# Optimization experiments

Measured on AMD Instinct MI355X. Metric: run time of the kernel, lower is better.

## Reference

```python
import jax, jax.numpy as jnp
import numpy as np

EMB_DIM = 128
WALK_LEN = 40
WINDOW = 5
NEG_SIZE = 5
NEG_WEIGHT = 1.0
NUM_NODES = 1_000_000
BATCH = 512


def _pair_indices(walk_length=WALK_LEN, window_size=WINDOW):
    # replicates the idx_list_src / idx_list_dst construction in __init__
    src, dst = [], []
    for i in range(walk_length):
        for j in range(max(0, i - window_size), i):
            src.append(j); dst.append(i)
        for j in range(i + 1, min(walk_length, i + 1 + window_size)):
            src.append(j); dst.append(i)
    return np.asarray(src, dtype=np.int64), np.asarray(dst, dtype=np.int64)

_SRC, _DST = _pair_indices()  # each has 370 entries
NUM_PAIRS = _SRC.shape[0]


def setup_inputs() -> dict:
    key = jax.random.key(0)
    k1, k2, k3, k4 = jax.random.split(key, 4)
    batch_walk = jax.random.randint(k1, (BATCH, WALK_LEN), 0, NUM_NODES, dtype=jnp.int64)
    neg_idx_dst = jax.random.randint(k2, (BATCH * NUM_PAIRS * NEG_SIZE,), 0, BATCH * WALK_LEN, dtype=jnp.int64)
    init_range = 1.0 / EMB_DIM
    node_embed = jax.random.normal(k3, (NUM_NODES, EMB_DIM), dtype=jnp.float32) * init_range
    context_embed = jax.random.normal(k4, (NUM_NODES, EMB_DIM), dtype=jnp.float32) * init_range
    return {"batch_walk": batch_walk, "neg_idx_dst": neg_idx_dst,
            "node_embed": node_embed, "context_embed": context_embed}


def reference(batch_walk, neg_idx_dst, node_embed, context_embed):
    B = batch_walk.shape[0]
    flat_walk = batch_walk.reshape(-1)                      # [B*L]
    batch_node = node_embed[flat_walk]                      # [B*L, D]
    batch_ctx = context_embed[flat_walk]                    # [B*L, D]

    offsets = (jnp.arange(B, dtype=jnp.int64) * WALK_LEN)[:, None]
    idx_src = (offsets + jnp.asarray(_SRC)[None, :]).reshape(-1)  # [B*370]
    idx_dst = (offsets + jnp.asarray(_DST)[None, :]).reshape(-1)  # [B*370]

    pos_src = batch_node[idx_src]
    pos_dst = batch_ctx[idx_dst]
    pos_score = jnp.clip(jnp.sum(pos_src * pos_dst, axis=1), -6.0, 6.0)
    pos_loss = jnp.mean(-jax.nn.log_sigmoid(pos_score))

    neg_idx_src = jnp.repeat(idx_dst, NEG_SIZE)             # [B*370*NEG]
    neg_src = batch_node[neg_idx_src]
    neg_dst = batch_ctx[neg_idx_dst]
    neg_score = jnp.clip(jnp.sum(neg_src * neg_dst, axis=1), -6.0, 6.0)
    neg_loss = jnp.mean(-jax.nn.log_sigmoid(-neg_score)) * NEG_SIZE * NEG_WEIGHT

    return pos_loss + neg_loss
```

## Files before the change

### kernel.cpp

```cpp
#include <hip/hip_runtime.h>
#include <hip/hip_fp16.h>

#define WALK_LEN 40
#define WINDOW   5
#define NPAIRS   370
#define BATCHSZ  512
#define NEGK     5
#define NPOS     (BATCHSZ * NPAIRS)
#define EMB      128
#define NQ       (BATCHSZ * WALK_LEN)
#define THREADS  512
#define GROUPS   (THREADS / 8)
#define HALFP    185
#define NBLOCKS  (BATCHSZ * 2)

struct PairTab { short src[NPAIRS]; short dst[NPAIRS]; };

constexpr PairTab make_pairs() {
    PairTab t{};
    int k = 0;
    for (int i = 0; i < WALK_LEN; ++i) {
        int lo = (i - WINDOW > 0) ? (i - WINDOW) : 0;
        for (int j = lo; j < i; ++j) { t.src[k] = (short)j; t.dst[k] = (short)i; ++k; }
        int hi = (i + 1 + WINDOW < WALK_LEN) ? (i + 1 + WINDOW) : WALK_LEN;
        for (int j = i + 1; j < hi; ++j) { t.src[k] = (short)j; t.dst[k] = (short)i; ++k; }
    }
    return t;
}

__constant__ PairTab g_pairs = make_pairs();

template <int CTRL>
__device__ __forceinline__ float dpp_add(float x) {
    int y = __builtin_amdgcn_update_dpp(0, __float_as_int(x), CTRL, 0xF, 0xF, true);
    return x + __int_as_float(y);
}
__device__ __forceinline__ float grp8_sum(float d) {
    d = dpp_add<0xB1>(d);
    d = dpp_add<0x4E>(d);
    d = dpp_add<0x141>(d);
    return d;
}

__device__ __forceinline__ float h2dot(uint4 A0, uint4 A1, uint4 C0, uint4 C1) {
    const __half2* a0 = (const __half2*)&A0;
    const __half2* a1 = (const __half2*)&A1;
    const __half2* c0 = (const __half2*)&C0;
    const __half2* c1 = (const __half2*)&C1;
    __half2 h0 = __float2half2_rn(0.f);
    __half2 h1 = __float2half2_rn(0.f);
    #pragma unroll
    for (int i = 0; i < 4; ++i) {
        h0 = __hfma2(a0[i], c0[i], h0);
        h1 = __hfma2(a1[i], c1[i], h1);
    }
    const __half2 hs = __hadd2(h0, h1);
    return __low2float(hs) + __high2float(hs);
}

__device__ __forceinline__ float clip6(float x) {
    return fminf(6.f, fmaxf(-6.f, x));
}

__global__ __launch_bounds__(256) void dw_gather(
    const int*   __restrict__ walk,
    const float* __restrict__ nodeE,
    const float* __restrict__ ctxE,
    unsigned short* __restrict__ dN,
    unsigned short* __restrict__ dC,
    float* __restrict__ out)
{
    if (blockIdx.x == 0 && threadIdx.x == 0) out[0] = 0.f;
    int idx = blockIdx.x * 256 + threadIdx.x;
    const int is_ctx = (idx >= NQ * 32);
    if (is_ctx) idx -= NQ * 32;
    const int q = idx >> 5, c = idx & 31;
    const int row = walk[q];
    const float* src = (is_ctx ? ctxE : nodeE) + (size_t)row * EMB;
    const float4 v = *((const float4*)src + c);
    ushort4 o;
    o.x = __half_as_ushort(__float2half(v.x));
    o.y = __half_as_ushort(__float2half(v.y));
    o.z = __half_as_ushort(__float2half(v.z));
    o.w = __half_as_ushort(__float2half(v.w));
    unsigned short* dst = (is_ctx ? dC : dN) + (size_t)q * EMB;
    *((ushort4*)dst + c) = o;
}

#define SLOT_DECL(S)                                                        \
    const int  jj##S = (S) * GROUPS + grp;                                  \
    const int  j##S  = jbase + ((jj##S < HALFP) ? jj##S : 0);               \
    const int* nb##S = negdst + ((size_t)b * NPAIRS + j##S) * NEGK;         \
    const int  qa##S = nb##S[0], qb##S = nb##S[1], qc##S = nb##S[2],        \
               qd##S = nb##S[3], qe##S = nb##S[4];                          \
    const uint4* ga##S = (const uint4*)(dC + (size_t)qa##S * EMB);          \
    const uint4* gb##S = (const uint4*)(dC + (size_t)qb##S * EMB);          \
    const uint4* gc##S = (const uint4*)(dC + (size_t)qc##S * EMB);          \
    const uint4* gd##S = (const uint4*)(dC + (size_t)qd##S * EMB);          \
    const uint4* ge##S = (const uint4*)(dC + (size_t)qe##S * EMB);          \
    const uint4 xa0##S = ga##S[lane8], xa1##S = ga##S[lane8 + 8];           \
    const uint4 xb0##S = gb##S[lane8], xb1##S = gb##S[lane8 + 8];           \
    const uint4 xc0##S = gc##S[lane8], xc1##S = gc##S[lane8 + 8];           \
    const uint4 xd0##S = gd##S[lane8], xd1##S = gd##S[lane8 + 8];           \
    const uint4 xe0##S = ge##S[lane8], xe1##S = ge##S[lane8 + 8];

#define SLOT_COMPUTE(S)                                                     \
    if (jj##S < HALFP) {                                                    \
        const int sj = g_pairs.src[j##S];                                   \
        const int dj = g_pairs.dst[j##S];                                   \
        const uint4* rN = (const uint4*)(sN + sj * 64);                     \
        const uint4* rC = (const uint4*)(sC + dj * 64);                     \
        const uint4* rS = (const uint4*)(sN + dj * 64);                     \
        const uint4 a0 = rN[lane8], a1 = rN[lane8 + 8];                     \
        const uint4 c0 = rC[lane8], c1 = rC[lane8 + 8];                     \
        const uint4 n0 = rS[lane8], n1 = rS[lane8 + 8];                     \
        const float sp = clip6(grp8_sum(h2dot(a0, a1, c0, c1)));            \
        const float s0 = clip6(grp8_sum(h2dot(n0, n1, xa0##S, xa1##S)));    \
        const float s1 = clip6(grp8_sum(h2dot(n0, n1, xb0##S, xb1##S)));    \
        const float s2 = clip6(grp8_sum(h2dot(n0, n1, xc0##S, xc1##S)));    \
        const float s3 = clip6(grp8_sum(h2dot(n0, n1, xd0##S, xd1##S)));    \
        const float s4 = clip6(grp8_sum(h2dot(n0, n1, xe0##S, xe1##S)));    \
        \
        const float p0 = (1.f + __expf(-sp)) * (1.f + __expf(s0));          \
        const float p1 = (1.f + __expf(s1))  * (1.f + __expf(s2));          \
        const float p2 = (1.f + __expf(s3))  * (1.f + __expf(s4));          \
        acc += __logf(p0 * p1 * p2);                                        \
    }

__global__ __launch_bounds__(THREADS, 2) void dw_score(
    const int* __restrict__ negdst,
    const unsigned short* __restrict__ dN,
    const unsigned short* __restrict__ dC,
    float* __restrict__ out)
{
    __shared__ unsigned int sN[WALK_LEN * 64];
    __shared__ unsigned int sC[WALK_LEN * 64];
    __shared__ float wsum[THREADS / 64];

    const int b    = blockIdx.x >> 1;
    const int half = blockIdx.x & 1;
    const int tid  = threadIdx.x;

    {
        const uint4* srcN = (const uint4*)(dN + (size_t)b * WALK_LEN * EMB);
        const uint4* srcC = (const uint4*)(dC + (size_t)b * WALK_LEN * EMB);
        for (int u = tid; u < WALK_LEN * 16; u += THREADS) {
            ((uint4*)sN)[u] = srcN[u];
            ((uint4*)sC)[u] = srcC[u];
        }
    }
    __syncthreads();

    const int lane8 = tid & 7;
    const int grp   = tid >> 3;
    const int jbase = half * HALFP;
    float acc = 0.0f;

    SLOT_DECL(0)
    SLOT_DECL(1)
    SLOT_DECL(2)
    SLOT_COMPUTE(0)
    SLOT_COMPUTE(1)
    SLOT_COMPUTE(2)

    acc += __shfl_xor(acc, 8);
    acc += __shfl_xor(acc, 16);
    acc += __shfl_xor(acc, 32);

    if ((tid & 63) == 0) wsum[tid >> 6] = acc;
    __syncthreads();
    if (tid == 0) {
        float tot = 0.f;
        #pragma unroll
        for (int w = 0; w < THREADS / 64; ++w) tot += wsum[w];
        atomicAdd(out, tot * (1.0f / (float)NPOS));
    }
}

extern "C" void kernel_launch(void* const* d_in, const int* in_sizes, int n_in,
                              void* d_out, int out_size, void* d_ws, size_t ws_size,
                              hipStream_t stream) {
    const int*   walk   = (const int*)d_in[0];
    const int*   negdst = (const int*)d_in[1];
    const float* nodeE  = (const float*)d_in[2];
    const float* ctxE   = (const float*)d_in[3];
    float*       out    = (float*)d_out;

    unsigned short* dN = (unsigned short*)d_ws;
    unsigned short* dC = dN + (size_t)NQ * EMB;

    dw_gather<<<(2 * NQ * 32) / 256, 256, 0, stream>>>(walk, nodeE, ctxE, dN, dC, out);
    dw_score<<<NBLOCKS, THREADS, 0, stream>>>(negdst, dN, dC, out);
}
```

Measured before the change: 38.15 us.

## Use 32-bit byte offsets and replace unrolled slot prefetch with a rolled loop

Computes addresses in both kernels as unsigned 32-bit byte offsets instead of 64-bit pointer arithmetic, which cuts address-computation instructions and VGPRs. It also swaps the three hoisted slot declarations, which issued all negative-row gathers up front, for a non-unrolled loop that loads and computes one slot per iteration. That lowers register pressure and can raise occupancy, but it gives up the cross-slot memory-level parallelism that hid gather latency.

```diff
diff --git a/kernel.cpp b/kernel.cpp
--- a/kernel.cpp
+++ b/kernel.cpp
@@ -62,6 +62,13 @@
     return fminf(6.f, fmaxf(-6.f, x));
 }
 
+__device__ __forceinline__ uint4 ldu4(const unsigned short* base, unsigned off) {
+    return *(const uint4*)((const char*)base + off);
+}
+__device__ __forceinline__ float4 ldf4(const float* base, unsigned off) {
+    return *(const float4*)((const char*)base + off);
+}
+
 __global__ __launch_bounds__(256) void dw_gather(
     const int*   __restrict__ walk,
     const float* __restrict__ nodeE,
@@ -75,57 +82,16 @@
     const int is_ctx = (idx >= NQ * 32);
     if (is_ctx) idx -= NQ * 32;
     const int q = idx >> 5, c = idx & 31;
-    const int row = walk[q];
-    const float* src = (is_ctx ? ctxE : nodeE) + (size_t)row * EMB;
-    const float4 v = *((const float4*)src + c);
+    const unsigned row = (unsigned)walk[q];
+    const float4 v = ldf4(is_ctx ? ctxE : nodeE, row * 512u + (unsigned)c * 16u);
     ushort4 o;
     o.x = __half_as_ushort(__float2half(v.x));
     o.y = __half_as_ushort(__float2half(v.y));
     o.z = __half_as_ushort(__float2half(v.z));
     o.w = __half_as_ushort(__float2half(v.w));
-    unsigned short* dst = (is_ctx ? dC : dN) + (size_t)q * EMB;
-    *((ushort4*)dst + c) = o;
+    unsigned short* dst = (is_ctx ? dC : dN);
+    *(ushort4*)((char*)dst + (unsigned)q * 256u + (unsigned)c * 8u) = o;
 }
-
-#define SLOT_DECL(S)                                                        \
-    const int  jj##S = (S) * GROUPS + grp;                                  \
-    const int  j##S  = jbase + ((jj##S < HALFP) ? jj##S : 0);               \
-    const int* nb##S = negdst + ((size_t)b * NPAIRS + j##S) * NEGK;         \
-    const int  qa##S = nb##S[0], qb##S = nb##S[1], qc##S = nb##S[2],        \
-               qd##S = nb##S[3], qe##S = nb##S[4];                          \
-    const uint4* ga##S = (const uint4*)(dC + (size_t)qa##S * EMB);          \
-    const uint4* gb##S = (const uint4*)(dC + (size_t)qb##S * EMB);          \
-    const uint4* gc##S = (const uint4*)(dC + (size_t)qc##S * EMB);          \
-    const uint4* gd##S = (const uint4*)(dC + (size_t)qd##S * EMB);          \
-    const uint4* ge##S = (const uint4*)(dC + (size_t)qe##S * EMB);          \
-    const uint4 xa0##S = ga##S[lane8], xa1##S = ga##S[lane8 + 8];           \
-    const uint4 xb0##S = gb##S[lane8], xb1##S = gb##S[lane8 + 8];           \
-    const uint4 xc0##S = gc##S[lane8], xc1##S = gc##S[lane8 + 8];           \
-    const uint4 xd0##S = gd##S[lane8], xd1##S = gd##S[lane8 + 8];           \
-    const uint4 xe0##S = ge##S[lane8], xe1##S = ge##S[lane8 + 8];
-
-#define SLOT_COMPUTE(S)                                                     \
-    if (jj##S < HALFP) {                                                    \
-        const int sj = g_pairs.src[j##S];                                   \
-        const int dj = g_pairs.dst[j##S];                                   \
-        const uint4* rN = (const uint4*)(sN + sj * 64);                     \
-        const uint4* rC = (const uint4*)(sC + dj * 64);                     \
-        const uint4* rS = (const uint4*)(sN + dj * 64);                     \
-        const uint4 a0 = rN[lane8], a1 = rN[lane8 + 8];                     \
-        const uint4 c0 = rC[lane8], c1 = rC[lane8 + 8];                     \
-        const uint4 n0 = rS[lane8], n1 = rS[lane8 + 8];                     \
-        const float sp = clip6(grp8_sum(h2dot(a0, a1, c0, c1)));            \
-        const float s0 = clip6(grp8_sum(h2dot(n0, n1, xa0##S, xa1##S)));    \
-        const float s1 = clip6(grp8_sum(h2dot(n0, n1, xb0##S, xb1##S)));    \
-        const float s2 = clip6(grp8_sum(h2dot(n0, n1, xc0##S, xc1##S)));    \
-        const float s3 = clip6(grp8_sum(h2dot(n0, n1, xd0##S, xd1##S)));    \
-        const float s4 = clip6(grp8_sum(h2dot(n0, n1, xe0##S, xe1##S)));    \
-        \
-        const float p0 = (1.f + __expf(-sp)) * (1.f + __expf(s0));          \
-        const float p1 = (1.f + __expf(s1))  * (1.f + __expf(s2));          \
-        const float p2 = (1.f + __expf(s3))  * (1.f + __expf(s4));          \
-        acc += __logf(p0 * p1 * p2);                                        \
-    }
 
 __global__ __launch_bounds__(THREADS, 2) void dw_score(
     const int* __restrict__ negdst,
@@ -142,11 +108,10 @@
     const int tid  = threadIdx.x;
 
     {
-        const uint4* srcN = (const uint4*)(dN + (size_t)b * WALK_LEN * EMB);
-        const uint4* srcC = (const uint4*)(dC + (size_t)b * WALK_LEN * EMB);
+        const unsigned base = (unsigned)b * (WALK_LEN * EMB * 2);
         for (int u = tid; u < WALK_LEN * 16; u += THREADS) {
-            ((uint4*)sN)[u] = srcN[u];
-            ((uint4*)sC)[u] = srcC[u];
+            ((uint4*)sN)[u] = ldu4(dN, base + (unsigned)u * 16u);
+            ((uint4*)sC)[u] = ldu4(dC, base + (unsigned)u * 16u);
         }
     }
     __syncthreads();
@@ -154,14 +119,49 @@
     const int lane8 = tid & 7;
     const int grp   = tid >> 3;
     const int jbase = half * HALFP;
+    const unsigned lo = (unsigned)lane8 * 16u;
     float acc = 0.0f;
 
-    SLOT_DECL(0)
-    SLOT_DECL(1)
-    SLOT_DECL(2)
-    SLOT_COMPUTE(0)
-    SLOT_COMPUTE(1)
-    SLOT_COMPUTE(2)
+    #pragma unroll 1
+    for (int it = 0; it < 3; ++it) {
+        const int jj = it * GROUPS + grp;
+        if (jj < HALFP) {
+            const int j = jbase + jj;
+            const unsigned p = (unsigned)b * NPAIRS + (unsigned)j;
+
+            const int* nb = (const int*)((const char*)negdst + p * 20u);
+            const unsigned q0 = (unsigned)nb[0], q1 = (unsigned)nb[1],
+                           q2 = (unsigned)nb[2], q3 = (unsigned)nb[3],
+                           q4 = (unsigned)nb[4];
+
+            const uint4 xa0 = ldu4(dC, q0 * 256u + lo), xa1 = ldu4(dC, q0 * 256u + lo + 128u);
+            const uint4 xb0 = ldu4(dC, q1 * 256u + lo), xb1 = ldu4(dC, q1 * 256u + lo + 128u);
+            const uint4 xc0 = ldu4(dC, q2 * 256u + lo), xc1 = ldu4(dC, q2 * 256u + lo + 128u);
+            const uint4 xd0 = ldu4(dC, q3 * 256u + lo), xd1 = ldu4(dC, q3 * 256u + lo + 128u);
+            const uint4 xe0 = ldu4(dC, q4 * 256u + lo), xe1 = ldu4(dC, q4 * 256u + lo + 128u);
+
+            const int sj = g_pairs.src[j];
+            const int dj = g_pairs.dst[j];
+            const uint4* rN = (const uint4*)(sN + sj * 64);
+            const uint4* rC = (const uint4*)(sC + dj * 64);
+            const uint4* rS = (const uint4*)(sN + dj * 64);
+            const uint4 a0 = rN[lane8], a1 = rN[lane8 + 8];
+            const uint4 c0 = rC[lane8], c1 = rC[lane8 + 8];
+            const uint4 n0 = rS[lane8], n1 = rS[lane8 + 8];
+
+            const float sp = clip6(grp8_sum(h2dot(a0, a1, c0, c1)));
+            const float s0 = clip6(grp8_sum(h2dot(n0, n1, xa0, xa1)));
+            const float s1 = clip6(grp8_sum(h2dot(n0, n1, xb0, xb1)));
+            const float s2 = clip6(grp8_sum(h2dot(n0, n1, xc0, xc1)));
+            const float s3 = clip6(grp8_sum(h2dot(n0, n1, xd0, xd1)));
+            const float s4 = clip6(grp8_sum(h2dot(n0, n1, xe0, xe1)));
+
+            const float p0 = (1.f + __expf(-sp)) * (1.f + __expf(s0));
+            const float p1 = (1.f + __expf(s1))  * (1.f + __expf(s2));
+            const float p2 = (1.f + __expf(s3))  * (1.f + __expf(s4));
+            acc += __logf(p0 * p1 * p2);
+        }
+    }
 
     acc += __shfl_xor(acc, 8);
     acc += __shfl_xor(acc, 16);
```

Result: no change. 37.85 us (-0.8%).
